# Kernel optimization log

Hardware: AMD Instinct MI355X
Metric: run time of the kernel (lower is better)

The kernel has to match this reference:

```python
import jax, jax.numpy as jnp
import numpy as np

IN_FEATURES = 4096
OUT_FEATURES = 16384
TOKENS = 32


def setup_inputs() -> dict:
    key = jax.random.key(0)
    k1, k2, k3, k4 = jax.random.split(key, 4)
    x = jax.random.normal(k1, (TOKENS, IN_FEATURES), dtype=jnp.float16)
    # int8-valued weights in [-127, 127]
    weight_int8 = jax.random.randint(k2, (OUT_FEATURES, IN_FEATURES), -127, 128, dtype=jnp.int32)
    # per-output-channel scale, positive (amax/127 in the original)
    scale = (jax.random.uniform(k3, (OUT_FEATURES,), dtype=jnp.float32) * 0.02 + 1e-4).astype(jnp.float16)
    bias = jax.random.normal(k4, (OUT_FEATURES,), dtype=jnp.float16)
    return {"x": x, "weight_int8": weight_int8, "scale": scale, "bias": bias}


def reference(x, weight_int8, scale, bias):
    # Dequantize int8 weights to compute dtype with per-row scale, then linear.
    w = weight_int8.astype(jnp.float16) * scale[:, None]          # [out, in] fp16
    return jnp.dot(x, w.T) + bias                                  # [tokens, out]
```

## Files before the change

kernel.cpp:

```cpp
#include <hip/hip_runtime.h>
#include <hip/hip_bf16.h>


typedef __attribute__((ext_vector_type(4))) int    i32x4;
typedef __attribute__((ext_vector_type(4))) float  f32x4;
typedef __attribute__((ext_vector_type(8))) short  s16x8;
typedef __attribute__((ext_vector_type(8))) __bf16 bf16x8;

constexpr int K = 4096;
constexpr int N = 16384;
constexpr int BKI = 1024;
constexpr int NT = K / BKI;
constexpr int PITCH = 4096 + 16;
constexpr size_t XB_OFF = 0;

__device__ inline unsigned short f2bf_rne(float f) {
    unsigned u = __builtin_bit_cast(unsigned, f);
    u += 0x7FFF + ((u >> 16) & 1);
    return (unsigned short)(u >> 16);
}

__device__ inline bf16x8 cvtW(i32x4 lo, i32x4 hi) {
    s16x8 r;
#pragma unroll
    for (int i = 0; i < 4; ++i) {
        r[i]     = (short)(__builtin_bit_cast(unsigned, (float)lo[i]) >> 16);
        r[i + 4] = (short)(__builtin_bit_cast(unsigned, (float)hi[i]) >> 16);
    }
    return __builtin_bit_cast(bf16x8, r);
}

__global__ __launch_bounds__(256) void xcvt_kernel(const float* __restrict__ x,
                                                   unsigned short* __restrict__ xb) {
    const int i = (blockIdx.x * 256 + threadIdx.x) * 8;
    f32x4 lo = *reinterpret_cast<const f32x4*>(x + i);
    f32x4 hi = *reinterpret_cast<const f32x4*>(x + i + 4);
    s16x8 r;
#pragma unroll
    for (int j = 0; j < 4; ++j) {
        r[j]     = (short)f2bf_rne(lo[j]);
        r[j + 4] = (short)f2bf_rne(hi[j]);
    }
    *reinterpret_cast<s16x8*>(xb + i) = r;
}

__global__ __launch_bounds__(256, 2) void w8gemm_kernel(
    const __bf16* __restrict__ xb,
    const int* __restrict__ w,
    const float* __restrict__ scale,
    const float* __restrict__ bias,
    float* __restrict__ out)
{
    extern __shared__ char smem[];

    const int tid  = threadIdx.x;
    const int lane = tid & 63;
    const int wave = tid >> 6;
    const int n16  = lane & 15;
    const int quad = lane >> 4;

    const int c0 = blockIdx.x * 16;

    auto stage = [&](int it) {
#pragma unroll
        for (int j = 0; j < 4; ++j) {
            const int row = wave * 4 + j;
            const char* gsrc = (const char*)(w + (size_t)(c0 + row) * K + it * BKI)
                               + (size_t)lane * 16;
            char* ldst = smem + row * PITCH + lane * 16;
#pragma unroll
            for (int s = 0; s < 4; ++s) {
                __builtin_amdgcn_global_load_lds(
                    (const __attribute__((address_space(1))) void*)(gsrc + s * 1024),
                    (__attribute__((address_space(3))) void*)(ldst + s * 1024),
                    16, 0, 0);
            }
        }
    };

    const char* lrow = smem + n16 * PITCH + quad * 32 + wave * 1024;
    const __bf16* __restrict__ xr0 = xb + (size_t)n16 * K + wave * 256 + quad * 8;
    const __bf16* __restrict__ xr1 = xr0 + (size_t)16 * K;

    f32x4 acc0 = {0.f, 0.f, 0.f, 0.f};
    f32x4 acc1 = {0.f, 0.f, 0.f, 0.f};

    stage(0);
#pragma unroll 1
    for (int it = 0; it < NT; ++it) {
        bf16x8 aX0[8], aX1[8];
#pragma unroll
        for (int j = 0; j < 8; ++j) {
            const int off = it * BKI + j * 32;
            aX0[j] = *reinterpret_cast<const bf16x8*>(xr0 + off);
            aX1[j] = *reinterpret_cast<const bf16x8*>(xr1 + off);
        }
        __syncthreads();
#pragma unroll
        for (int j = 0; j < 8; ++j) {
            i32x4 b0 = *reinterpret_cast<const i32x4*>(lrow + j * 128);
            i32x4 b1 = *reinterpret_cast<const i32x4*>(lrow + j * 128 + 16);
            bf16x8 bf = cvtW(b0, b1);
            acc0 = __builtin_amdgcn_mfma_f32_16x16x32_bf16(aX0[j], bf, acc0, 0, 0, 0);
            acc1 = __builtin_amdgcn_mfma_f32_16x16x32_bf16(aX1[j], bf, acc1, 0, 0, 0);
        }
        __syncthreads();
        if (it + 1 < NT) stage(it + 1);
    }

    __syncthreads();
    float* red = (float*)smem;
#pragma unroll
    for (int v = 0; v < 4; ++v) {
        red[wave * 512 + lane * 8 + v]     = acc0[v];
        red[wave * 512 + lane * 8 + 4 + v] = acc1[v];
    }
    __syncthreads();
#pragma unroll
    for (int pp = 0; pp < 2; ++pp) {
        const int p = tid + pp * 256;
        float s = red[p] + red[512 + p] + red[1024 + p] + red[1536 + p];
        const int pl   = p >> 3;
        const int r    = p & 7;
        const int half = r >> 2;
        const int v    = r & 3;
        const int pn   = pl & 15;
        const int pq   = pl >> 4;
        const int token = half * 16 + pq * 4 + v;
        const int c = c0 + pn;
        out[(size_t)token * N + c] = s * scale[c] + bias[c];
    }
}

extern "C" void kernel_launch(void* const* d_in, const int* in_sizes, int n_in,
                              void* d_out, int out_size, void* d_ws, size_t ws_size,
                              hipStream_t stream) {
    const float* x     = (const float*)d_in[0];
    const int*   w     = (const int*)d_in[1];
    const float* scale = (const float*)d_in[2];
    const float* bias  = (const float*)d_in[3];
    float* out = (float*)d_out;

    unsigned short* xb = (unsigned short*)((char*)d_ws + XB_OFF);

    xcvt_kernel<<<dim3(64), dim3(256), 0, stream>>>(x, xb);
    w8gemm_kernel<<<dim3(N / 16), dim3(256), 16 * PITCH, stream>>>(
        (const __bf16*)xb, w, scale, bias, out);
}
```

Before: 369.6 us.

## Shrink GEMV tile to 4 output channels with register-staged full-row loads

Each block now handles 4 output channels instead of 16, so the grid grows from 1024 to 4096 blocks. All 4×4096 int32 weights per block are loaded at once through registers with nontemporal loads, stored to LDS, and consumed after a single barrier, replacing the pipelined global_load_lds stages. The MFMA tile stays 16 wide, so 12 of 16 lanes feed zeros and three quarters of the matrix work is wasted. In exchange the weight stream gets more memory-level parallelism and fewer barriers.

After: 435.2 us. 17.8% more time.

```diff
diff --git a/kernel.cpp b/kernel.cpp
--- a/kernel.cpp
+++ b/kernel.cpp
@@ -9,9 +9,7 @@
 
 constexpr int K = 4096;
 constexpr int N = 16384;
-constexpr int BKI = 1024;
-constexpr int NT = K / BKI;
-constexpr int PITCH = 4096 + 16;
+constexpr int RPITCH = 16384 + 16;
 constexpr size_t XB_OFF = 0;
 
 __device__ inline unsigned short f2bf_rne(float f) {
@@ -59,53 +57,49 @@
     const int n16  = lane & 15;
     const int quad = lane >> 4;
 
-    const int c0 = blockIdx.x * 16;
+    const int c0 = blockIdx.x * 4;
 
-    auto stage = [&](int it) {
+    const char* gb = (const char*)(w + (size_t)c0 * K);
+    i32x4 stg[16];
 #pragma unroll
-        for (int j = 0; j < 4; ++j) {
-            const int row = wave * 4 + j;
-            const char* gsrc = (const char*)(w + (size_t)(c0 + row) * K + it * BKI)
-                               + (size_t)lane * 16;
-            char* ldst = smem + row * PITCH + lane * 16;
+    for (int r = 0; r < 16; ++r)
+        stg[r] = __builtin_nontemporal_load(
+            reinterpret_cast<const i32x4*>(gb + r * 4096 + tid * 16));
 #pragma unroll
-            for (int s = 0; s < 4; ++s) {
-                __builtin_amdgcn_global_load_lds(
-                    (const __attribute__((address_space(1))) void*)(gsrc + s * 1024),
-                    (__attribute__((address_space(3))) void*)(ldst + s * 1024),
-                    16, 0, 0);
-            }
-        }
-    };
+    for (int r = 0; r < 16; ++r)
+        *reinterpret_cast<i32x4*>(smem + (r >> 2) * RPITCH + (r & 3) * 4096
+                                  + tid * 16) = stg[r];
+    __syncthreads();
 
-    const char* lrow = smem + n16 * PITCH + quad * 32 + wave * 1024;
-    const __bf16* __restrict__ xr0 = xb + (size_t)n16 * K + wave * 256 + quad * 8;
+    const char* lrow = smem + n16 * RPITCH + wave * 4096 + quad * 32;
+    const __bf16* __restrict__ xr0 = xb + (size_t)n16 * K + wave * 1024 + quad * 8;
     const __bf16* __restrict__ xr1 = xr0 + (size_t)16 * K;
 
     f32x4 acc0 = {0.f, 0.f, 0.f, 0.f};
     f32x4 acc1 = {0.f, 0.f, 0.f, 0.f};
+    const bool act = (n16 < 4);
 
-    stage(0);
 #pragma unroll 1
-    for (int it = 0; it < NT; ++it) {
+    for (int jt = 0; jt < 4; ++jt) {
         bf16x8 aX0[8], aX1[8];
 #pragma unroll
         for (int j = 0; j < 8; ++j) {
-            const int off = it * BKI + j * 32;
+            const int off = jt * 256 + j * 32;
             aX0[j] = *reinterpret_cast<const bf16x8*>(xr0 + off);
             aX1[j] = *reinterpret_cast<const bf16x8*>(xr1 + off);
         }
-        __syncthreads();
 #pragma unroll
         for (int j = 0; j < 8; ++j) {
-            i32x4 b0 = *reinterpret_cast<const i32x4*>(lrow + j * 128);
-            i32x4 b1 = *reinterpret_cast<const i32x4*>(lrow + j * 128 + 16);
+            i32x4 b0 = {0, 0, 0, 0};
+            i32x4 b1 = {0, 0, 0, 0};
+            if (act) {
+                b0 = *reinterpret_cast<const i32x4*>(lrow + (jt * 8 + j) * 128);
+                b1 = *reinterpret_cast<const i32x4*>(lrow + (jt * 8 + j) * 128 + 16);
+            }
             bf16x8 bf = cvtW(b0, b1);
             acc0 = __builtin_amdgcn_mfma_f32_16x16x32_bf16(aX0[j], bf, acc0, 0, 0, 0);
             acc1 = __builtin_amdgcn_mfma_f32_16x16x32_bf16(aX1[j], bf, acc1, 0, 0, 0);
         }
-        __syncthreads();
-        if (it + 1 < NT) stage(it + 1);
     }
 
     __syncthreads();
@@ -116,18 +110,15 @@
         red[wave * 512 + lane * 8 + 4 + v] = acc1[v];
     }
     __syncthreads();
-#pragma unroll
-    for (int pp = 0; pp < 2; ++pp) {
-        const int p = tid + pp * 256;
-        float s = red[p] + red[512 + p] + red[1024 + p] + red[1536 + p];
-        const int pl   = p >> 3;
-        const int r    = p & 7;
-        const int half = r >> 2;
-        const int v    = r & 3;
-        const int pn   = pl & 15;
-        const int pq   = pl >> 4;
-        const int token = half * 16 + pq * 4 + v;
-        const int c = c0 + pn;
+    if (tid < 128) {
+        const int ch    = tid & 3;
+        const int token = tid >> 2;
+        const int half  = token >> 4;
+        const int q     = (token >> 2) & 3;
+        const int v     = token & 3;
+        const int slot  = (q * 16 + ch) * 8 + half * 4 + v;
+        float s = red[slot] + red[512 + slot] + red[1024 + slot] + red[1536 + slot];
+        const int c = c0 + ch;
         out[(size_t)token * N + c] = s * scale[c] + bias[c];
     }
 }
@@ -144,6 +135,6 @@
     unsigned short* xb = (unsigned short*)((char*)d_ws + XB_OFF);
 
     xcvt_kernel<<<dim3(64), dim3(256), 0, stream>>>(x, xb);
-    w8gemm_kernel<<<dim3(N / 16), dim3(256), 16 * PITCH, stream>>>(
+    w8gemm_kernel<<<dim3(N / 4), dim3(256), 4 * RPITCH, stream>>>(
         (const __bf16*)xb, w, scale, bias, out);
 }
```
